# Performance work log

Hardware: AMD Instinct MI355X
Metric: run time of the kernel (lower is better)

## Reference

```python
import jax, jax.numpy as jnp
import numpy as np

N_NODES = 50000
N_EDGES = 800000


def _deg_inv_sqrt(idx, n):
    deg = jax.ops.segment_sum(jnp.ones(idx.shape[0], jnp.float32), idx, num_segments=n)
    return jnp.power(jnp.clip(deg, 1.0, None), -0.5)


def _gcn_layer(x, W, b, src, dst, out_norm, in_norm, n):
    # left degree norm, dense matmul, gather-scatter-sum over edges, right norm, bias
    h = (x * out_norm[:, None]) @ W
    agg = jax.ops.segment_sum(h[src], dst, num_segments=n)
    return agg * in_norm[:, None] + b


def setup_inputs() -> dict:
    key = jax.random.key(0)
    ks = jax.random.split(key, 8)
    def xavier(k, fi, fo):
        a = np.sqrt(6.0 / (fi + fo))
        return jax.random.uniform(k, (fi, fo), jnp.float32, -a, a)
    x = jax.random.normal(ks[0], (N_NODES, 256), jnp.float32)
    edge_index = jax.random.randint(ks[1], (2, N_EDGES), 0, N_NODES, dtype=jnp.int64)
    return {
        "x": x,
        "edge_index": edge_index,
        "W0": xavier(ks[2], 256, 128), "b0": jnp.zeros((128,), jnp.float32),
        "W1": xavier(ks[3], 128, 128), "b1": jnp.zeros((128,), jnp.float32),
        "W2": xavier(ks[4], 128, 128), "b2": jnp.zeros((128,), jnp.float32),
        "W3": xavier(ks[5], 128, 64),  "b3": jnp.zeros((64,), jnp.float32),
    }


def reference(x, edge_index, W0, b0, W1, b1, W2, b2, W3, b3):
    n = x.shape[0]
    src, dst = edge_index[0], edge_index[1]
    out_norm = _deg_inv_sqrt(src, n)  # out-degree based (src side)
    in_norm = _deg_inv_sqrt(dst, n)   # in-degree based (dst side)
    Ws = [W0, W1, W2, W3]
    bs = [b0, b1, b2, b3]
    h = x
    for i in range(4):
        h = _gcn_layer(h, Ws[i], bs[i], src, dst, out_norm, in_norm, n)
        if i < 3:  # relu on all but final layer
            h = jax.nn.relu(h)
    return h
```

## Files before the change

### kernel.cpp

```cpp
#include <hip/hip_runtime.h>
#include <hip/hip_fp16.h>


typedef __attribute__((ext_vector_type(8))) short short8;
typedef __attribute__((ext_vector_type(4))) float f32x4;

#define NRANGE 8
#define NCHUNK 64
#define RMAX   6272

__device__ inline unsigned short bf16_rne(float v) {
    union { float f; unsigned u; } c; c.f = v;
    unsigned u = c.u;
    unsigned lsb = (u >> 16) & 1u;
    u += 0x7fffu + lsb;
    return (unsigned short)(u >> 16);
}
__device__ inline float bf16_to_f(unsigned short h) {
    union { unsigned u; float f; } c; c.u = ((unsigned)h) << 16;
    return c.f;
}
__device__ inline void split_bf16(float v, unsigned short& hi, unsigned short& lo) {
    hi = bf16_rne(v);
    lo = bf16_rne(v - bf16_to_f(hi));
}


__global__ __launch_bounds__(256) void k_hist(const int* __restrict__ src,
                                              const int* __restrict__ dst,
                                              int ne, int R, int E,
                                              int* __restrict__ cnt_s,
                                              int* __restrict__ cnt_d,
                                              int* __restrict__ pos) {
    __shared__ int hs[RMAX];
    __shared__ int hd[RMAX];
    int r = blockIdx.x & (NRANGE - 1);
    int c = blockIdx.x >> 3;
    int tid = threadIdx.x;
    for (int i = tid; i < R; i += 256) { hs[i] = 0; hd[i] = 0; }
    __syncthreads();
    int lo = r * R, hi = lo + R;
    int e0 = c * E, e1 = min(e0 + E, ne);
    for (int i = e0 + tid; i < e1; i += 256) {
        int s = src[i], d = dst[i];
        if (s >= lo && s < hi) atomicAdd(&hs[s - lo], 1);
        if (d >= lo && d < hi) {
            int p = atomicAdd(&hd[d - lo], 1);
            pos[i] = p;
        }
    }
    __syncthreads();
    int base = (r * NCHUNK + c) * R;
    for (int i = tid; i < R; i += 256) {
        cnt_s[base + i] = hs[i];
        cnt_d[base + i] = hd[i];
    }
}

__global__ void k_reduce_norms(const int* __restrict__ cnt_s,
                               const int* __restrict__ cnt_d, int R, int n,
                               float* __restrict__ onrm, float* __restrict__ inrm,
                               int* __restrict__ degd_sum) {
    int i = blockIdx.x * blockDim.x + threadIdx.x;
    if (i >= NRANGE * R) return;
    int r = i / R, ip = i - r * R;
    int ds = 0, dd = 0;
    for (int c = 0; c < NCHUNK; ++c) {
        ds += cnt_s[(r * NCHUNK + c) * R + ip];
        dd += cnt_d[(r * NCHUNK + c) * R + ip];
    }
    degd_sum[i] = dd;
    if (i < n) {
        onrm[i] = rsqrtf((float)max(ds, 1));
        inrm[i] = rsqrtf((float)max(dd, 1));
    }
}

__global__ __launch_bounds__(1024) void k_scan(const int* __restrict__ deg, int n,
                                               int* __restrict__ row_ptr) {
    __shared__ int wsum[16];
    __shared__ int carry;
    int tid = threadIdx.x;
    int lane = tid & 63;
    int wid = tid >> 6;
    if (tid == 0) carry = 0;
    __syncthreads();
    int n4 = (n + 3) >> 2;
    for (int base = 0; base < n4; base += 1024) {
        int i4 = base + tid;
        int4 v = make_int4(0, 0, 0, 0);
        if (i4 < n4) v = ((const int4*)deg)[i4];
        int s = v.x + v.y + v.z + v.w;
        int x = s;
#pragma unroll
        for (int off = 1; off < 64; off <<= 1) {
            int y = __shfl_up(x, off, 64);
            if (lane >= off) x += y;
        }
        if (lane == 63) wsum[wid] = x;
        __syncthreads();
        if (wid == 0 && lane < 16) {
            int w = wsum[lane];
#pragma unroll
            for (int off = 1; off < 16; off <<= 1) {
                int y = __shfl_up(w, off, 16);
                if (lane >= off) w += y;
            }
            wsum[lane] = w;
        }
        __syncthreads();
        int excl = x - s + carry + (wid > 0 ? wsum[wid - 1] : 0);
        if (i4 < n4) {
            int e0 = excl, e1 = e0 + v.x, e2 = e1 + v.y, e3 = e2 + v.z;
            ((int4*)row_ptr)[i4] = make_int4(e0, e1, e2, e3);
        }
        __syncthreads();
        if (tid == 0) carry += wsum[15];
        __syncthreads();
    }
    if (tid == 0) row_ptr[n] = carry;
}

__global__ void k_cursors(const int* __restrict__ row_ptr,
                          const int* __restrict__ cnt_d, int R, int n,
                          int* __restrict__ cbase) {
    int i = blockIdx.x * blockDim.x + threadIdx.x;
    if (i >= NRANGE * R) return;
    int r = i / R, ip = i - r * R;
    int run = (i < n) ? row_ptr[i] : 0;
    for (int c = 0; c < NCHUNK; ++c) {
        int idx = (r * NCHUNK + c) * R + ip;
        cbase[idx] = run;
        run += cnt_d[idx];
    }
}

__global__ void k_csr_scatter(const int* __restrict__ src,
                              const int* __restrict__ dst,
                              const int* __restrict__ pos,
                              const int* __restrict__ cbase,
                              int ne, int R, int E,
                              int* __restrict__ eidx) {
    int i = blockIdx.x * blockDim.x + threadIdx.x;
    if (i >= ne) return;
    int d = dst[i];
    int r = d / R, ip = d - r * R;
    int c = i / E;
    eidx[cbase[(r * NCHUNK + c) * R + ip] + pos[i]] = src[i];
}


__global__ __launch_bounds__(256) void k_split_x(const float* __restrict__ x,
                                                 const float* __restrict__ onrm,
                                                 unsigned short* __restrict__ Ah,
                                                 unsigned short* __restrict__ Al, int n) {
    int i4 = blockIdx.x * blockDim.x + threadIdx.x;
    int row = i4 >> 6;
    if (row >= n) return;
    float4 v = ((const float4*)x)[i4];
    float s = onrm[row];
    unsigned short h0, l0, h1, l1, h2, l2, h3, l3;
    split_bf16(v.x * s, h0, l0);
    split_bf16(v.y * s, h1, l1);
    split_bf16(v.z * s, h2, l2);
    split_bf16(v.w * s, h3, l3);
    ushort4 hv, lv;
    hv.x = h0; hv.y = h1; hv.z = h2; hv.w = h3;
    lv.x = l0; lv.y = l1; lv.z = l2; lv.w = l3;
    ((ushort4*)Ah)[i4] = hv;
    ((ushort4*)Al)[i4] = lv;
}

__global__ void k_split_w_all(const float* __restrict__ W0, const float* __restrict__ W1,
                              const float* __restrict__ W2, const float* __restrict__ W3,
                              unsigned short* __restrict__ Wh0, unsigned short* __restrict__ Wl0,
                              unsigned short* __restrict__ Wh1, unsigned short* __restrict__ Wl1,
                              unsigned short* __restrict__ Wh2, unsigned short* __restrict__ Wl2,
                              unsigned short* __restrict__ Wh3, unsigned short* __restrict__ Wl3) {
    int i = blockIdx.x * blockDim.x + threadIdx.x;
    const float* W; unsigned short *Wh, *Wl; int K, F, off;
    if (i < 32768)                    { W = W0; Wh = Wh0; Wl = Wl0; K = 256; F = 128; off = i; }
    else if (i < 32768 + 16384)       { W = W1; Wh = Wh1; Wl = Wl1; K = 128; F = 128; off = i - 32768; }
    else if (i < 32768 + 32768)       { W = W2; Wh = Wh2; Wl = Wl2; K = 128; F = 128; off = i - 49152; }
    else if (i < 32768 + 32768 + 8192){ W = W3; Wh = Wh3; Wl = Wl3; K = 128; F = 64;  off = i - 65536; }
    else return;
    int k = off / F, c = off % F;
    unsigned short h, l;
    split_bf16(W[k * F + c], h, l);
    Wh[c * K + k] = h;
    Wl[c * K + k] = l;
}

template <int K, int N>
__global__ __launch_bounds__(256) void k_mm(const unsigned short* __restrict__ Ah,
                                            const unsigned short* __restrict__ Al,
                                            const unsigned short* __restrict__ Bh,
                                            const unsigned short* __restrict__ Bl,
                                            __half* __restrict__ H, int n) {
    constexpr int KT = 128;
    constexpr int NT = N / 16;
    constexpr int NKT = K / KT;
    __shared__ unsigned short sBh[N * KT];
    __shared__ unsigned short sBl[N * KT];

    int tid = threadIdx.x;
    int w = tid >> 6, lane = tid & 63;
    int quad = lane >> 4, l16 = lane & 15;
    int row_base = blockIdx.x * 128 + w * 32;

    int ar0 = row_base + l16;
    int ar1 = row_base + 16 + l16;
    if (ar0 >= n) ar0 = n - 1;
    if (ar1 >= n) ar1 = n - 1;

    f32x4 acc[2][NT];
#pragma unroll
    for (int m = 0; m < 2; ++m)
#pragma unroll
        for (int t = 0; t < NT; ++t) acc[m][t] = (f32x4){0.f, 0.f, 0.f, 0.f};

    for (int kt = 0; kt < NKT; ++kt) {
        if (kt) __syncthreads();
        for (int idx = tid; idx < N * 16; idx += 256) {
            int c = idx >> 4;
            int g = idx & 15;
            short8 vh = *(const short8*)(Bh + (size_t)c * K + kt * KT + g * 8);
            short8 vl = *(const short8*)(Bl + (size_t)c * K + kt * KT + g * 8);
            int sg = g ^ (c & 15);
            *(short8*)(&sBh[c * KT + sg * 8]) = vh;
            *(short8*)(&sBl[c * KT + sg * 8]) = vl;
        }
        __syncthreads();

        const unsigned short* a0h = Ah + (size_t)ar0 * K + kt * KT;
        const unsigned short* a0l = Al + (size_t)ar0 * K + kt * KT;
        const unsigned short* a1h = Ah + (size_t)ar1 * K + kt * KT;
        const unsigned short* a1l = Al + (size_t)ar1 * K + kt * KT;

#pragma unroll
        for (int k0 = 0; k0 < KT; k0 += 32) {
            int eoff = k0 + quad * 8;
            short8 a0hv = *(const short8*)(a0h + eoff);
            short8 a0lv = *(const short8*)(a0l + eoff);
            short8 a1hv = *(const short8*)(a1h + eoff);
            short8 a1lv = *(const short8*)(a1l + eoff);
            int g = (k0 >> 3) + quad;
            int sg8 = (g ^ l16) * 8;
#pragma unroll
            for (int t = 0; t < NT; ++t) {
                int cb = (t * 16 + l16) * KT;
                short8 bh = *(const short8*)(&sBh[cb + sg8]);
                short8 bl = *(const short8*)(&sBl[cb + sg8]);
                acc[0][t] = __builtin_amdgcn_mfma_f32_16x16x32_bf16(a0hv, bh, acc[0][t], 0, 0, 0);
                acc[0][t] = __builtin_amdgcn_mfma_f32_16x16x32_bf16(a0lv, bh, acc[0][t], 0, 0, 0);
                acc[0][t] = __builtin_amdgcn_mfma_f32_16x16x32_bf16(a0hv, bl, acc[0][t], 0, 0, 0);
                acc[1][t] = __builtin_amdgcn_mfma_f32_16x16x32_bf16(a1hv, bh, acc[1][t], 0, 0, 0);
                acc[1][t] = __builtin_amdgcn_mfma_f32_16x16x32_bf16(a1lv, bh, acc[1][t], 0, 0, 0);
                acc[1][t] = __builtin_amdgcn_mfma_f32_16x16x32_bf16(a1hv, bl, acc[1][t], 0, 0, 0);
            }
        }
    }

#pragma unroll
    for (int m = 0; m < 2; ++m) {
#pragma unroll
        for (int t = 0; t < NT; ++t) {
#pragma unroll
            for (int r = 0; r < 4; ++r) {
                int grow = row_base + m * 16 + quad * 4 + r;
                if (grow < n) H[(size_t)grow * N + t * 16 + l16] = __float2half(acc[m][t][r]);
            }
        }
    }
}


__global__ __launch_bounds__(256) void k_agg128_split(const __half* __restrict__ h,
                                                      const int* __restrict__ row_ptr,
                                                      const int* __restrict__ eidx,
                                                      const float* __restrict__ inrm,
                                                      const float* __restrict__ onrm,
                                                      const float* __restrict__ bias,
                                                      unsigned short* __restrict__ Ah,
                                                      unsigned short* __restrict__ Al, int n) {
    int wave = threadIdx.x >> 6;
    int lane = threadIdx.x & 63;
    int half = lane >> 5;
    int l = lane & 31;
    int node = blockIdx.x * 8 + wave * 2 + half;
    bool valid = node < n;
    int nd = valid ? node : n - 1;
    int beg = row_ptr[nd], end = row_ptr[nd + 1];
    const ushort4* h4 = (const ushort4*)h;

    float a0[8], a1[8], a2[8], a3[8];
#pragma unroll
    for (int u = 0; u < 8; ++u) { a0[u] = 0.f; a1[u] = 0.f; a2[u] = 0.f; a3[u] = 0.f; }
    int j = beg;
    for (; j + 8 <= end; j += 8) {
        int s[8];
#pragma unroll
        for (int u = 0; u < 8; ++u) s[u] = eidx[j + u];
        ushort4 v[8];
#pragma unroll
        for (int u = 0; u < 8; ++u) v[u] = h4[(size_t)s[u] * 32 + l];
#pragma unroll
        for (int u = 0; u < 8; ++u) {
            __half2* ph = reinterpret_cast<__half2*>(&v[u]);
            float2 f0 = __half22float2(ph[0]);
            float2 f1 = __half22float2(ph[1]);
            a0[u] += f0.x; a1[u] += f0.y; a2[u] += f1.x; a3[u] += f1.y;
        }
    }
    for (; j < end; ++j) {
        ushort4 v = h4[(size_t)eidx[j] * 32 + l];
        __half2* ph = reinterpret_cast<__half2*>(&v);
        float2 f0 = __half22float2(ph[0]);
        float2 f1 = __half22float2(ph[1]);
        a0[0] += f0.x; a1[0] += f0.y; a2[0] += f1.x; a3[0] += f1.y;
    }
    float s0 = ((a0[0] + a0[1]) + (a0[2] + a0[3])) + ((a0[4] + a0[5]) + (a0[6] + a0[7]));
    float s1 = ((a1[0] + a1[1]) + (a1[2] + a1[3])) + ((a1[4] + a1[5]) + (a1[6] + a1[7]));
    float s2 = ((a2[0] + a2[1]) + (a2[2] + a2[3])) + ((a2[4] + a2[5]) + (a2[6] + a2[7]));
    float s3 = ((a3[0] + a3[1]) + (a3[2] + a3[3])) + ((a3[4] + a3[5]) + (a3[6] + a3[7]));

    float nrm = inrm[nd];
    float on = onrm[nd];
    float4 b4 = ((const float4*)bias)[l];
    float o0 = fmaxf(s0 * nrm + b4.x, 0.f) * on;
    float o1 = fmaxf(s1 * nrm + b4.y, 0.f) * on;
    float o2 = fmaxf(s2 * nrm + b4.z, 0.f) * on;
    float o3 = fmaxf(s3 * nrm + b4.w, 0.f) * on;
    ushort4 hv, lv;
    split_bf16(o0, hv.x, lv.x);
    split_bf16(o1, hv.y, lv.y);
    split_bf16(o2, hv.z, lv.z);
    split_bf16(o3, hv.w, lv.w);
    if (valid) {
        ((ushort4*)Ah)[(size_t)node * 32 + l] = hv;
        ((ushort4*)Al)[(size_t)node * 32 + l] = lv;
    }
}

__global__ __launch_bounds__(256) void k_agg64(const __half* __restrict__ h,
                                               const int* __restrict__ row_ptr,
                                               const int* __restrict__ eidx,
                                               const float* __restrict__ inrm,
                                               const float* __restrict__ bias,
                                               float* __restrict__ out, int n) {
    int wave = threadIdx.x >> 6;
    int lane = threadIdx.x & 63;
    int half = lane >> 5;
    int l = lane & 31;
    int node = blockIdx.x * 8 + wave * 2 + half;
    bool valid = node < n;
    int nd = valid ? node : n - 1;
    int beg = row_ptr[nd], end = row_ptr[nd + 1];
    const __half2* h2 = (const __half2*)h;

    float a0[8], a1[8];
#pragma unroll
    for (int u = 0; u < 8; ++u) { a0[u] = 0.f; a1[u] = 0.f; }
    int j = beg;
    for (; j + 8 <= end; j += 8) {
        int s[8];
#pragma unroll
        for (int u = 0; u < 8; ++u) s[u] = eidx[j + u];
        __half2 v[8];
#pragma unroll
        for (int u = 0; u < 8; ++u) v[u] = h2[(size_t)s[u] * 32 + l];
#pragma unroll
        for (int u = 0; u < 8; ++u) {
            float2 f = __half22float2(v[u]);
            a0[u] += f.x; a1[u] += f.y;
        }
    }
    for (; j < end; ++j) {
        float2 f = __half22float2(h2[(size_t)eidx[j] * 32 + l]);
        a0[0] += f.x; a1[0] += f.y;
    }
    float s0 = ((a0[0] + a0[1]) + (a0[2] + a0[3])) + ((a0[4] + a0[5]) + (a0[6] + a0[7]));
    float s1 = ((a1[0] + a1[1]) + (a1[2] + a1[3])) + ((a1[4] + a1[5]) + (a1[6] + a1[7]));

    float nrm = inrm[nd];
    float2 b2 = ((const float2*)bias)[l];
    float2 o;
    o.x = s0 * nrm + b2.x;
    o.y = s1 * nrm + b2.y;
    if (valid) ((float2*)out)[(size_t)node * 32 + l] = o;
}

template <int K, int FO, int TX, int TY, int RPT>
__global__ __launch_bounds__(256) void k_matmul(const float* __restrict__ X,
                                                const float* __restrict__ W,
                                                const float* __restrict__ onrm,
                                                float* __restrict__ H, int n) {
    constexpr int BROWS = TY * RPT;
    constexpr int LDK = K + 1;
    __shared__ float xs[BROWS * LDK];
    int tx = threadIdx.x, ty = threadIdx.y;
    int tid = ty * TX + tx;
    int row0 = blockIdx.x * BROWS;

    for (int idx = tid; idx < BROWS * K; idx += 256) {
        int r = idx / K;
        int k = idx - r * K;
        int row = row0 + r;
        xs[r * LDK + k] = (row < n) ? X[(size_t)row * K + k] : 0.f;
    }
    __syncthreads();

    float4 acc[RPT];
#pragma unroll
    for (int r = 0; r < RPT; ++r) acc[r] = make_float4(0.f, 0.f, 0.f, 0.f);

    const float4* W4 = (const float4*)W;
#pragma unroll 4
    for (int k = 0; k < K; ++k) {
        float4 w = W4[k * (FO / 4) + tx];
#pragma unroll
        for (int r = 0; r < RPT; ++r) {
            float xv = xs[(ty * RPT + r) * LDK + k];
            acc[r].x += xv * w.x;
            acc[r].y += xv * w.y;
            acc[r].z += xv * w.z;
            acc[r].w += xv * w.w;
        }
    }

#pragma unroll
    for (int r = 0; r < RPT; ++r) {
        int row = row0 + ty * RPT + r;
        if (row < n) {
            float s = onrm[row];
            float4 o = make_float4(acc[r].x * s, acc[r].y * s, acc[r].z * s, acc[r].w * s);
            ((float4*)H)[(size_t)row * (FO / 4) + tx] = o;
        }
    }
}

__global__ __launch_bounds__(256) void k_agg128f(const float* __restrict__ h,
                                                 const int* __restrict__ row_ptr,
                                                 const int* __restrict__ eidx,
                                                 const float* __restrict__ inrm,
                                                 const float* __restrict__ bias,
                                                 float* __restrict__ out, int n, int relu) {
    int node = blockIdx.x * 4 + (threadIdx.x >> 6);
    int lane = threadIdx.x & 63;
    if (node >= n) return;
    int beg = row_ptr[node], end = row_ptr[node + 1];
    const float2* h2 = (const float2*)h;
    float ax = 0.f, ay = 0.f;
    for (int j = beg; j < end; ++j) {
        int s = eidx[j];
        float2 v = h2[(size_t)s * 64 + lane];
        ax += v.x;
        ay += v.y;
    }
    float nrm = inrm[node];
    float2 b2 = ((const float2*)bias)[lane];
    float ox = ax * nrm + b2.x;
    float oy = ay * nrm + b2.y;
    if (relu) { ox = fmaxf(ox, 0.f); oy = fmaxf(oy, 0.f); }
    float2 o; o.x = ox; o.y = oy;
    ((float2*)out)[(size_t)node * 64 + lane] = o;
}

__global__ __launch_bounds__(256) void k_agg64f(const float* __restrict__ h,
                                                const int* __restrict__ row_ptr,
                                                const int* __restrict__ eidx,
                                                const float* __restrict__ inrm,
                                                const float* __restrict__ bias,
                                                float* __restrict__ out, int n) {
    int node = blockIdx.x * 4 + (threadIdx.x >> 6);
    int lane = threadIdx.x & 63;
    if (node >= n) return;
    int beg = row_ptr[node], end = row_ptr[node + 1];
    float acc = 0.f;
    for (int j = beg; j < end; ++j) {
        int s = eidx[j];
        acc += h[(size_t)s * 64 + lane];
    }
    out[(size_t)node * 64 + lane] = acc * inrm[node] + bias[lane];
}

__global__ void k_degrees_leg(const int* __restrict__ src, const int* __restrict__ dst,
                              int ne, int* __restrict__ degs, int* __restrict__ degd) {
    int i = blockIdx.x * blockDim.x + threadIdx.x;
    if (i < ne) {
        atomicAdd(&degs[src[i]], 1);
        atomicAdd(&degd[dst[i]], 1);
    }
}
__global__ void k_norms_leg(const int* __restrict__ degs, const int* __restrict__ degd,
                            float* __restrict__ onrm, float* __restrict__ inrm,
                            int* __restrict__ degd_sum, int n) {
    int i = blockIdx.x * blockDim.x + threadIdx.x;
    if (i < n) {
        degd_sum[i] = degd[i];
        onrm[i] = rsqrtf((float)max(degs[i], 1));
        inrm[i] = rsqrtf((float)max(degd[i], 1));
    }
}
__global__ void k_copy_int(const int* __restrict__ a, int* __restrict__ b, int n) {
    int i = blockIdx.x * blockDim.x + threadIdx.x;
    if (i < n) b[i] = a[i];
}
__global__ void k_build_csr_leg(const int* __restrict__ src, const int* __restrict__ dst,
                                int ne, int* __restrict__ cursor, int* __restrict__ eidx) {
    int i = blockIdx.x * blockDim.x + threadIdx.x;
    if (i < ne) {
        int p = atomicAdd(&cursor[dst[i]], 1);
        eidx[p] = src[i];
    }
}

static inline size_t align_up(size_t v, size_t a) { return (v + a - 1) & ~(a - 1); }

extern "C" void kernel_launch(void* const* d_in, const int* in_sizes, int n_in,
                              void* d_out, int out_size, void* d_ws, size_t ws_size,
                              hipStream_t stream) {
    const float* x  = (const float*)d_in[0];
    const int* ei   = (const int*)d_in[1];
    const float* W0 = (const float*)d_in[2];
    const float* b0 = (const float*)d_in[3];
    const float* W1 = (const float*)d_in[4];
    const float* b1 = (const float*)d_in[5];
    const float* W2 = (const float*)d_in[6];
    const float* b2 = (const float*)d_in[7];
    const float* W3 = (const float*)d_in[8];
    const float* b3 = (const float*)d_in[9];

    const int n  = in_sizes[0] / 256;
    const int ne = in_sizes[1] / 2;
    const int n_pad = (n + 127) & ~127;
    const int* src = ei;
    const int* dst = ei + ne;

    char* ws = (char*)d_ws;
    size_t off = 0;
    auto take = [&](size_t bytes) { void* p = ws + off; off = align_up(off + bytes, 256); return p; };
    int* row_ptr  = (int*)take((size_t)(n_pad + 4) * 4);
    int* degd_sum = (int*)take((size_t)n_pad * 4);
    int* eidx     = (int*)take((size_t)ne * 4);
    float* onrm   = (float*)take((size_t)n * 4);
    float* inrm   = (float*)take((size_t)n * 4);

    size_t off_save = off;
    unsigned short* Ah  = (unsigned short*)take((size_t)n_pad * 256 * 2);
    unsigned short* Al  = (unsigned short*)take((size_t)n_pad * 256 * 2);
    __half* hbuf        = (__half*)take((size_t)n * 128 * 2);
    unsigned short* Wh0 = (unsigned short*)take(256 * 128 * 2);
    unsigned short* Wl0 = (unsigned short*)take(256 * 128 * 2);
    unsigned short* Wh1 = (unsigned short*)take(128 * 128 * 2);
    unsigned short* Wl1 = (unsigned short*)take(128 * 128 * 2);
    unsigned short* Wh2 = (unsigned short*)take(128 * 128 * 2);
    unsigned short* Wl2 = (unsigned short*)take(128 * 128 * 2);
    unsigned short* Wh3 = (unsigned short*)take(128 * 64 * 2);
    unsigned short* Wl3 = (unsigned short*)take(128 * 64 * 2);
    bool use_mfma = (off <= ws_size);

    char* pre = (char*)Ah;
    const int R = ((n + NRANGE * 64 - 1) / (NRANGE * 64)) * 64;
    const size_t cntSz = align_up((size_t)NRANGE * NCHUNK * R * 4, 256);
    int* cnt_s = (int*)pre;
    int* cnt_d = (int*)(pre + cntSz);
    int* cbase = (int*)(pre + 2 * cntSz);
    int* pos   = (int*)(pre + 3 * cntSz);

    const int aggGrid = (n + 7) / 8;

    if (R <= RMAX) {
        const int E = (ne + NCHUNK - 1) / NCHUNK;
        k_hist<<<NRANGE * NCHUNK, 256, 0, stream>>>(src, dst, ne, R, E, cnt_s, cnt_d, pos);
        k_reduce_norms<<<(NRANGE * R + 255) / 256, 256, 0, stream>>>(cnt_s, cnt_d, R, n,
                                                                     onrm, inrm, degd_sum);
        k_scan<<<1, 1024, 0, stream>>>(degd_sum, n, row_ptr);
        k_cursors<<<(NRANGE * R + 255) / 256, 256, 0, stream>>>(row_ptr, cnt_d, R, n, cbase);
        k_csr_scatter<<<(ne + 255) / 256, 256, 0, stream>>>(src, dst, pos, cbase, ne, R, E, eidx);
    } else {
        int* degs   = cnt_s;
        int* degd   = cnt_s + n_pad;
        int* cursor = cnt_s + 2 * n_pad;
        hipMemsetAsync(degs, 0, (size_t)2 * n_pad * 4, stream);
        k_degrees_leg<<<(ne + 255) / 256, 256, 0, stream>>>(src, dst, ne, degs, degd);
        k_norms_leg<<<(n + 255) / 256, 256, 0, stream>>>(degs, degd, onrm, inrm, degd_sum, n);
        k_scan<<<1, 1024, 0, stream>>>(degd_sum, n, row_ptr);
        k_copy_int<<<(n + 255) / 256, 256, 0, stream>>>(row_ptr, cursor, n);
        k_build_csr_leg<<<(ne + 255) / 256, 256, 0, stream>>>(src, dst, ne, cursor, eidx);
    }

    if (use_mfma) {
        k_split_w_all<<<(73728 + 255) / 256, 256, 0, stream>>>(
            W0, W1, W2, W3, Wh0, Wl0, Wh1, Wl1, Wh2, Wl2, Wh3, Wl3);
        k_split_x<<<((n * 64) + 255) / 256, 256, 0, stream>>>(x, onrm, Ah, Al, n);

        const int mmGrid = n_pad / 128;
        k_mm<256, 128><<<mmGrid, 256, 0, stream>>>(Ah, Al, Wh0, Wl0, hbuf, n);
        k_agg128_split<<<aggGrid, 256, 0, stream>>>(hbuf, row_ptr, eidx, inrm, onrm, b0, Ah, Al, n);
        k_mm<128, 128><<<mmGrid, 256, 0, stream>>>(Ah, Al, Wh1, Wl1, hbuf, n);
        k_agg128_split<<<aggGrid, 256, 0, stream>>>(hbuf, row_ptr, eidx, inrm, onrm, b1, Ah, Al, n);
        k_mm<128, 128><<<mmGrid, 256, 0, stream>>>(Ah, Al, Wh2, Wl2, hbuf, n);
        k_agg128_split<<<aggGrid, 256, 0, stream>>>(hbuf, row_ptr, eidx, inrm, onrm, b2, Ah, Al, n);
        k_mm<128, 64><<<mmGrid, 256, 0, stream>>>(Ah, Al, Wh3, Wl3, hbuf, n);
        k_agg64<<<aggGrid, 256, 0, stream>>>(hbuf, row_ptr, eidx, inrm, b3, (float*)d_out, n);
    } else {
        off = off_save;
        float* hbufF  = (float*)take((size_t)n * 128 * 4);
        float* xnextF = (float*)take((size_t)n * 128 * 4);
        const int aggGridF = (n + 3) / 4;

        k_matmul<256, 128, 32, 8, 4><<<(n + 31) / 32, dim3(32, 8), 0, stream>>>(x, W0, onrm, hbufF, n);
        k_agg128f<<<aggGridF, 256, 0, stream>>>(hbufF, row_ptr, eidx, inrm, b0, xnextF, n, 1);
        k_matmul<128, 128, 32, 8, 4><<<(n + 31) / 32, dim3(32, 8), 0, stream>>>(xnextF, W1, onrm, hbufF, n);
        k_agg128f<<<aggGridF, 256, 0, stream>>>(hbufF, row_ptr, eidx, inrm, b1, xnextF, n, 1);
        k_matmul<128, 128, 32, 8, 4><<<(n + 31) / 32, dim3(32, 8), 0, stream>>>(xnextF, W2, onrm, hbufF, n);
        k_agg128f<<<aggGridF, 256, 0, stream>>>(hbufF, row_ptr, eidx, inrm, b2, xnextF, n, 1);
        k_matmul<128, 64, 16, 16, 4><<<(n + 63) / 64, dim3(16, 16), 0, stream>>>(xnextF, W3, onrm, hbufF, n);
        k_agg64f<<<aggGridF, 256, 0, stream>>>(hbufF, row_ptr, eidx, inrm, b3, (float*)d_out, n);
    }
}
```

Before: 382.4 us.

## Fuse input bf16 split into first matmul and widen aggregation gathers to 16B

```diff
diff --git a/kernel.cpp b/kernel.cpp
--- a/kernel.cpp
+++ b/kernel.cpp
@@ -150,27 +150,6 @@
 }
 
 
-__global__ __launch_bounds__(256) void k_split_x(const float* __restrict__ x,
-                                                 const float* __restrict__ onrm,
-                                                 unsigned short* __restrict__ Ah,
-                                                 unsigned short* __restrict__ Al, int n) {
-    int i4 = blockIdx.x * blockDim.x + threadIdx.x;
-    int row = i4 >> 6;
-    if (row >= n) return;
-    float4 v = ((const float4*)x)[i4];
-    float s = onrm[row];
-    unsigned short h0, l0, h1, l1, h2, l2, h3, l3;
-    split_bf16(v.x * s, h0, l0);
-    split_bf16(v.y * s, h1, l1);
-    split_bf16(v.z * s, h2, l2);
-    split_bf16(v.w * s, h3, l3);
-    ushort4 hv, lv;
-    hv.x = h0; hv.y = h1; hv.z = h2; hv.w = h3;
-    lv.x = l0; lv.y = l1; lv.z = l2; lv.w = l3;
-    ((ushort4*)Ah)[i4] = hv;
-    ((ushort4*)Al)[i4] = lv;
-}
-
 __global__ void k_split_w_all(const float* __restrict__ W0, const float* __restrict__ W1,
                               const float* __restrict__ W2, const float* __restrict__ W3,
                               unsigned short* __restrict__ Wh0, unsigned short* __restrict__ Wl0,
@@ -191,9 +170,11 @@
     Wl[c * K + k] = l;
 }
 
-template <int K, int N>
+template <int K, int N, bool FA>
 __global__ __launch_bounds__(256) void k_mm(const unsigned short* __restrict__ Ah,
                                             const unsigned short* __restrict__ Al,
+                                            const float* __restrict__ Xf,
+                                            const float* __restrict__ onrm,
                                             const unsigned short* __restrict__ Bh,
                                             const unsigned short* __restrict__ Bl,
                                             __half* __restrict__ H, int n) {
@@ -212,6 +193,9 @@
     int ar1 = row_base + 16 + l16;
     if (ar0 >= n) ar0 = n - 1;
     if (ar1 >= n) ar1 = n - 1;
+
+    float on0 = 0.f, on1 = 0.f;
+    if (FA) { on0 = onrm[ar0]; on1 = onrm[ar1]; }
 
     f32x4 acc[2][NT];
 #pragma unroll
@@ -232,18 +216,33 @@
         }
         __syncthreads();
 
-        const unsigned short* a0h = Ah + (size_t)ar0 * K + kt * KT;
-        const unsigned short* a0l = Al + (size_t)ar0 * K + kt * KT;
-        const unsigned short* a1h = Ah + (size_t)ar1 * K + kt * KT;
-        const unsigned short* a1l = Al + (size_t)ar1 * K + kt * KT;
-
 #pragma unroll
         for (int k0 = 0; k0 < KT; k0 += 32) {
             int eoff = k0 + quad * 8;
-            short8 a0hv = *(const short8*)(a0h + eoff);
-            short8 a0lv = *(const short8*)(a0l + eoff);
-            short8 a1hv = *(const short8*)(a1h + eoff);
-            short8 a1lv = *(const short8*)(a1l + eoff);
+            short8 a0hv, a0lv, a1hv, a1lv;
+            if (FA) {
+                const float* x0 = Xf + (size_t)ar0 * K + kt * KT + eoff;
+                const float* x1 = Xf + (size_t)ar1 * K + kt * KT + eoff;
+                float4 p00 = *(const float4*)x0;
+                float4 p01 = *(const float4*)(x0 + 4);
+                float4 p10 = *(const float4*)x1;
+                float4 p11 = *(const float4*)(x1 + 4);
+                float e0[8] = {p00.x, p00.y, p00.z, p00.w, p01.x, p01.y, p01.z, p01.w};
+                float e1[8] = {p10.x, p10.y, p10.z, p10.w, p11.x, p11.y, p11.z, p11.w};
+#pragma unroll
+                for (int q = 0; q < 8; ++q) {
+                    unsigned short hh, ll;
+                    split_bf16(e0[q] * on0, hh, ll);
+                    a0hv[q] = (short)hh; a0lv[q] = (short)ll;
+                    split_bf16(e1[q] * on1, hh, ll);
+                    a1hv[q] = (short)hh; a1lv[q] = (short)ll;
+                }
+            } else {
+                a0hv = *(const short8*)(Ah + (size_t)ar0 * K + kt * KT + eoff);
+                a0lv = *(const short8*)(Al + (size_t)ar0 * K + kt * KT + eoff);
+                a1hv = *(const short8*)(Ah + (size_t)ar1 * K + kt * KT + eoff);
+                a1lv = *(const short8*)(Al + (size_t)ar1 * K + kt * KT + eoff);
+            }
             int g = (k0 >> 3) + quad;
             int sg8 = (g ^ l16) * 8;
 #pragma unroll
@@ -285,60 +284,68 @@
                                                       unsigned short* __restrict__ Al, int n) {
     int wave = threadIdx.x >> 6;
     int lane = threadIdx.x & 63;
-    int half = lane >> 5;
-    int l = lane & 31;
-    int node = blockIdx.x * 8 + wave * 2 + half;
+    int g = lane >> 4;
+    int l = lane & 15;
+    int node = blockIdx.x * 16 + wave * 4 + g;
     bool valid = node < n;
     int nd = valid ? node : n - 1;
     int beg = row_ptr[nd], end = row_ptr[nd + 1];
-    const ushort4* h4 = (const ushort4*)h;
-
-    float a0[8], a1[8], a2[8], a3[8];
-#pragma unroll
-    for (int u = 0; u < 8; ++u) { a0[u] = 0.f; a1[u] = 0.f; a2[u] = 0.f; a3[u] = 0.f; }
+    const short8* h8 = (const short8*)h;
+
+    float a[4][8];
+#pragma unroll
+    for (int u = 0; u < 4; ++u)
+#pragma unroll
+        for (int c = 0; c < 8; ++c) a[u][c] = 0.f;
+
     int j = beg;
-    for (; j + 8 <= end; j += 8) {
-        int s[8];
-#pragma unroll
-        for (int u = 0; u < 8; ++u) s[u] = eidx[j + u];
-        ushort4 v[8];
-#pragma unroll
-        for (int u = 0; u < 8; ++u) v[u] = h4[(size_t)s[u] * 32 + l];
-#pragma unroll
-        for (int u = 0; u < 8; ++u) {
-            __half2* ph = reinterpret_cast<__half2*>(&v[u]);
-            float2 f0 = __half22float2(ph[0]);
-            float2 f1 = __half22float2(ph[1]);
-            a0[u] += f0.x; a1[u] += f0.y; a2[u] += f1.x; a3[u] += f1.y;
+    for (; j + 4 <= end; j += 4) {
+        int s[4];
+#pragma unroll
+        for (int u = 0; u < 4; ++u) s[u] = eidx[j + u];
+        short8 v[4];
+#pragma unroll
+        for (int u = 0; u < 4; ++u) v[u] = h8[(size_t)s[u] * 16 + l];
+#pragma unroll
+        for (int u = 0; u < 4; ++u) {
+            const __half2* ph = reinterpret_cast<const __half2*>(&v[u]);
+#pragma unroll
+            for (int p = 0; p < 4; ++p) {
+                float2 f = __half22float2(ph[p]);
+                a[u][2 * p] += f.x;
+                a[u][2 * p + 1] += f.y;
+            }
         }
     }
     for (; j < end; ++j) {
-        ushort4 v = h4[(size_t)eidx[j] * 32 + l];
-        __half2* ph = reinterpret_cast<__half2*>(&v);
-        float2 f0 = __half22float2(ph[0]);
-        float2 f1 = __half22float2(ph[1]);
-        a0[0] += f0.x; a1[0] += f0.y; a2[0] += f1.x; a3[0] += f1.y;
-    }
-    float s0 = ((a0[0] + a0[1]) + (a0[2] + a0[3])) + ((a0[4] + a0[5]) + (a0[6] + a0[7]));
-    float s1 = ((a1[0] + a1[1]) + (a1[2] + a1[3])) + ((a1[4] + a1[5]) + (a1[6] + a1[7]));
-    float s2 = ((a2[0] + a2[1]) + (a2[2] + a2[3])) + ((a2[4] + a2[5]) + (a2[6] + a2[7]));
-    float s3 = ((a3[0] + a3[1]) + (a3[2] + a3[3])) + ((a3[4] + a3[5]) + (a3[6] + a3[7]));
+        short8 v = h8[(size_t)eidx[j] * 16 + l];
+        const __half2* ph = reinterpret_cast<const __half2*>(&v);
+#pragma unroll
+        for (int p = 0; p < 4; ++p) {
+            float2 f = __half22float2(ph[p]);
+            a[0][2 * p] += f.x;
+            a[0][2 * p + 1] += f.y;
+        }
+    }
 
     float nrm = inrm[nd];
     float on = onrm[nd];
-    float4 b4 = ((const float4*)bias)[l];
-    float o0 = fmaxf(s0 * nrm + b4.x, 0.f) * on;
-    float o1 = fmaxf(s1 * nrm + b4.y, 0.f) * on;
-    float o2 = fmaxf(s2 * nrm + b4.z, 0.f) * on;
-    float o3 = fmaxf(s3 * nrm + b4.w, 0.f) * on;
-    ushort4 hv, lv;
-    split_bf16(o0, hv.x, lv.x);
-    split_bf16(o1, hv.y, lv.y);
-    split_bf16(o2, hv.z, lv.z);
-    split_bf16(o3, hv.w, lv.w);
+    float4 b0 = ((const float4*)bias)[l * 2];
+    float4 b1 = ((const float4*)bias)[l * 2 + 1];
+    float bb[8] = {b0.x, b0.y, b0.z, b0.w, b1.x, b1.y, b1.z, b1.w};
+    short8 hv, lv;
+#pragma unroll
+    for (int c = 0; c < 8; ++c) {
+        float s = (a[0][c] + a[1][c]) + (a[2][c] + a[3][c]);
+        float o = fmaxf(s * nrm + bb[c], 0.f) * on;
+        unsigned short hh, ll;
+        split_bf16(o, hh, ll);
+        hv[c] = (short)hh;
+        lv[c] = (short)ll;
+    }
     if (valid) {
-        ((ushort4*)Ah)[(size_t)node * 32 + l] = hv;
-        ((ushort4*)Al)[(size_t)node * 32 + l] = lv;
+        ((short8*)Ah)[(size_t)node * 16 + l] = hv;
+        ((short8*)Al)[(size_t)node * 16 + l] = lv;
     }
 }
 
@@ -350,44 +357,56 @@
                                                float* __restrict__ out, int n) {
     int wave = threadIdx.x >> 6;
     int lane = threadIdx.x & 63;
-    int half = lane >> 5;
-    int l = lane & 31;
-    int node = blockIdx.x * 8 + wave * 2 + half;
+    int g = lane >> 4;
+    int l = lane & 15;
+    int node = blockIdx.x * 16 + wave * 4 + g;
     bool valid = node < n;
     int nd = valid ? node : n - 1;
     int beg = row_ptr[nd], end = row_ptr[nd + 1];
-    const __half2* h2 = (const __half2*)h;
-
-    float a0[8], a1[8];
-#pragma unroll
-    for (int u = 0; u < 8; ++u) { a0[u] = 0.f; a1[u] = 0.f; }
+    const ushort4* h4 = (const ushort4*)h;
+
+    float a[8][4];
+#pragma unroll
+    for (int u = 0; u < 8; ++u)
+#pragma unroll
+        for (int c = 0; c < 4; ++c) a[u][c] = 0.f;
+
     int j = beg;
     for (; j + 8 <= end; j += 8) {
         int s[8];
 #pragma unroll
         for (int u = 0; u < 8; ++u) s[u] = eidx[j + u];
-        __half2 v[8];
-#pragma unroll
-        for (int u = 0; u < 8; ++u) v[u] = h2[(size_t)s[u] * 32 + l];
+        ushort4 v[8];
+#pragma unroll
+        for (int u = 0; u < 8; ++u) v[u] = h4[(size_t)s[u] * 16 + l];
 #pragma unroll
         for (int u = 0; u < 8; ++u) {
-            float2 f = __half22float2(v[u]);
-            a0[u] += f.x; a1[u] += f.y;
+            const __half2* ph = reinterpret_cast<const __half2*>(&v[u]);
+            float2 f0 = __half22float2(ph[0]);
+            float2 f1 = __half22float2(ph[1]);
+            a[u][0] += f0.x; a[u][1] += f0.y; a[u][2] += f1.x; a[u][3] += f1.y;
         }
     }
     for (; j < end; ++j) {
-        float2 f = __half22float2(h2[(size_t)eidx[j] * 32 + l]);
-        a0[0] += f.x; a1[0] += f.y;
-    }
-    float s0 = ((a0[0] + a0[1]) + (a0[2] + a0[3])) + ((a0[4] + a0[5]) + (a0[6] + a0[7]));
-    float s1 = ((a1[0] + a1[1]) + (a1[2] + a1[3])) + ((a1[4] + a1[5]) + (a1[6] + a1[7]));
+        ushort4 v = h4[(size_t)eidx[j] * 16 + l];
+        const __half2* ph = reinterpret_cast<const __half2*>(&v);
+        float2 f0 = __half22float2(ph[0]);
+        float2 f1 = __half22float2(ph[1]);
+        a[0][0] += f0.x; a[0][1] += f0.y; a[0][2] += f1.x; a[0][3] += f1.y;
+    }
 
     float nrm = inrm[nd];
-    float2 b2 = ((const float2*)bias)[l];
-    float2 o;
-    o.x = s0 * nrm + b2.x;
-    o.y = s1 * nrm + b2.y;
-    if (valid) ((float2*)out)[(size_t)node * 32 + l] = o;
+    float4 b4 = ((const float4*)bias)[l];
+    float4 o;
+    float s0 = ((a[0][0] + a[1][0]) + (a[2][0] + a[3][0])) + ((a[4][0] + a[5][0]) + (a[6][0] + a[7][0]));
+    float s1 = ((a[0][1] + a[1][1]) + (a[2][1] + a[3][1])) + ((a[4][1] + a[5][1]) + (a[6][1] + a[7][1]));
+    float s2 = ((a[0][2] + a[1][2]) + (a[2][2] + a[3][2])) + ((a[4][2] + a[5][2]) + (a[6][2] + a[7][2]));
+    float s3 = ((a[0][3] + a[1][3]) + (a[2][3] + a[3][3])) + ((a[4][3] + a[5][3]) + (a[6][3] + a[7][3]));
+    o.x = s0 * nrm + b4.x;
+    o.y = s1 * nrm + b4.y;
+    o.z = s2 * nrm + b4.z;
+    o.w = s3 * nrm + b4.w;
+    if (valid) ((float4*)out)[(size_t)node * 16 + l] = o;
 }
 
 template <int K, int FO, int TX, int TY, int RPT>
@@ -568,7 +587,7 @@
     int* cbase = (int*)(pre + 2 * cntSz);
     int* pos   = (int*)(pre + 3 * cntSz);
 
-    const int aggGrid = (n + 7) / 8;
+    const int aggGrid = (n + 15) / 16;
 
     if (R <= RMAX) {
         const int E = (ne + NCHUNK - 1) / NCHUNK;
@@ -593,16 +612,15 @@
     if (use_mfma) {
         k_split_w_all<<<(73728 + 255) / 256, 256, 0, stream>>>(
             W0, W1, W2, W3, Wh0, Wl0, Wh1, Wl1, Wh2, Wl2, Wh3, Wl3);
-        k_split_x<<<((n * 64) + 255) / 256, 256, 0, stream>>>(x, onrm, Ah, Al, n);
 
         const int mmGrid = n_pad / 128;
-        k_mm<256, 128><<<mmGrid, 256, 0, stream>>>(Ah, Al, Wh0, Wl0, hbuf, n);
+        k_mm<256, 128, true><<<mmGrid, 256, 0, stream>>>(nullptr, nullptr, x, onrm, Wh0, Wl0, hbuf, n);
         k_agg128_split<<<aggGrid, 256, 0, stream>>>(hbuf, row_ptr, eidx, inrm, onrm, b0, Ah, Al, n);
-        k_mm<128, 128><<<mmGrid, 256, 0, stream>>>(Ah, Al, Wh1, Wl1, hbuf, n);
+        k_mm<128, 128, false><<<mmGrid, 256, 0, stream>>>(Ah, Al, nullptr, nullptr, Wh1, Wl1, hbuf, n);
         k_agg128_split<<<aggGrid, 256, 0, stream>>>(hbuf, row_ptr, eidx, inrm, onrm, b1, Ah, Al, n);
-        k_mm<128, 128><<<mmGrid, 256, 0, stream>>>(Ah, Al, Wh2, Wl2, hbuf, n);
+        k_mm<128, 128, false><<<mmGrid, 256, 0, stream>>>(Ah, Al, nullptr, nullptr, Wh2, Wl2, hbuf, n);
         k_agg128_split<<<aggGrid, 256, 0, stream>>>(hbuf, row_ptr, eidx, inrm, onrm, b2, Ah, Al, n);
-        k_mm<128, 64><<<mmGrid, 256, 0, stream>>>(Ah, Al, Wh3, Wl3, hbuf, n);
+        k_mm<128, 64, false><<<mmGrid, 256, 0, stream>>>(Ah, Al, nullptr, nullptr, Wh3, Wl3, hbuf, n);
         k_agg64<<<aggGrid, 256, 0, stream>>>(hbuf, row_ptr, eidx, inrm, b3, (float*)d_out, n);
     } else {
         off = off_save;
```

Result: faster. 359.1 us (-6.1%).
